# Kernel tuning notes

Measured on AMD Instinct MI355X. Metric: run time of the kernel, lower is better.

The kernel has to match this reference:

```python
import jax, jax.numpy as jnp
import numpy as np

N_NODES = 50000


def _degree_norm(src, dst, n):
    # symmetric GCN normalization with self-loops already appended
    deg = jax.ops.segment_sum(jnp.ones(src.shape[0], jnp.float32), dst, num_segments=n)
    dinv = jnp.where(deg > 0, jax.lax.rsqrt(deg), 0.0)
    return dinv[src] * dinv[dst]  # [E_full]


def _gcn_layer(x, W, b, src, dst, norm, n):
    h = x @ W                                  # [N, out]
    msgs = h[src] * norm[:, None]              # gather + scale, [E_full, out]
    out = jax.ops.segment_sum(msgs, dst, num_segments=n)
    return out + b


def setup_inputs() -> dict:
    key = jax.random.key(0)
    k1, k2, k3, k4 = jax.random.split(key, 4)
    n, e, d_in, d_out = N_NODES, 800000, 256, 128
    x = jax.random.normal(k1, (n, d_in), jnp.float32)
    edge_index = jax.random.randint(k2, (2, e), 0, n, dtype=jnp.int64)
    W1 = jax.random.normal(k3, (d_in, 2 * d_out), jnp.float32) / np.sqrt(d_in)
    b1 = jnp.zeros((2 * d_out,), jnp.float32)
    W2 = jax.random.normal(k4, (2 * d_out, d_out), jnp.float32) / np.sqrt(2 * d_out)
    b2 = jnp.zeros((d_out,), jnp.float32)
    return {"x": x, "edge_index": edge_index, "W1": W1, "b1": b1, "W2": W2, "b2": b2}


def reference(x, edge_index, W1, b1, W2, b2):
    n = x.shape[0]
    loops = jnp.arange(n, dtype=edge_index.dtype)
    src = jnp.concatenate([edge_index[0], loops])
    dst = jnp.concatenate([edge_index[1], loops])
    norm = _degree_norm(src, dst, n)
    h = jax.nn.relu(_gcn_layer(x, W1, b1, src, dst, norm, n))
    h = jax.nn.relu(_gcn_layer(h, W2, b2, src, dst, norm, n))
    return h
```

## Files before the change

kernel.cpp:

```cpp
#include <hip/hip_runtime.h>
#include <hip/hip_bf16.h>


typedef __attribute__((ext_vector_type(8))) short bf16x8;
typedef __attribute__((ext_vector_type(4))) float f32x4;

__device__ inline float bf2f(unsigned short u) {
    return __uint_as_float(((unsigned)u) << 16);
}
__device__ inline unsigned short f2bf(float f) {
    unsigned x = __float_as_uint(f);
    unsigned r = (x + 0x7fffu + ((x >> 16) & 1u)) >> 16;
    return (unsigned short)r;
}
__device__ inline float bflo(unsigned u) { return __uint_as_float(u << 16); }
__device__ inline float bfhi(unsigned u) { return __uint_as_float(u & 0xffff0000u); }

__global__ void degree_kernel(const int* __restrict__ dst, unsigned* __restrict__ deg, int E) {
    int e = blockIdx.x * blockDim.x + threadIdx.x;
    if (e < E) atomicAdd(&deg[dst[e]], 1u);
}

__global__ void dinv_kernel(const unsigned* __restrict__ deg, float* __restrict__ dinv, int N) {
    int i = blockIdx.x * blockDim.x + threadIdx.x;
    if (i < N) dinv[i] = rsqrtf((float)(deg[i] + 1u));
}

__global__ __launch_bounds__(1024) void scan_kernel(const unsigned* __restrict__ deg,
                                                    int* __restrict__ rowptr,
                                                    int* __restrict__ cursor, int N) {
    __shared__ int wsum[16];
    __shared__ int carry_s;
    const int t = threadIdx.x, lane = t & 63, w = t >> 6;
    if (t == 0) carry_s = 0;
    __syncthreads();
    for (int base = 0; base < N; base += 4096) {
        int i0 = base + t * 4;
        int v[4];
#pragma unroll
        for (int j = 0; j < 4; j++) {
            int i = i0 + j;
            v[j] = (i < N) ? (int)deg[i] : 0;
        }
        int s = v[0] + v[1] + v[2] + v[3];
        int x = s;
#pragma unroll
        for (int off = 1; off < 64; off <<= 1) {
            int y = __shfl_up(x, off, 64);
            if (lane >= off) x += y;
        }
        if (lane == 63) wsum[w] = x;
        __syncthreads();
        if (w == 0 && lane < 16) {
            int ss = wsum[lane];
#pragma unroll
            for (int off = 1; off < 16; off <<= 1) {
                int y = __shfl_up(ss, off, 16);
                if ((lane & 15) >= off) ss += y;
            }
            wsum[lane] = ss;
        }
        __syncthreads();
        int waveoff = (w == 0) ? 0 : wsum[w - 1];
        int c = carry_s;
        int run = c + waveoff + (x - s);
#pragma unroll
        for (int j = 0; j < 4; j++) {
            int i = i0 + j;
            if (i < N) { rowptr[i] = run; cursor[i] = run; }
            run += v[j];
        }
        __syncthreads();
        if (t == 1023) carry_s = c + waveoff + x;
        __syncthreads();
    }
    if (t == 0) rowptr[N] = carry_s;
}

__global__ __launch_bounds__(256) void fill_kernel(const int* __restrict__ src,
                                                   const int* __restrict__ dst,
                                                   const float* __restrict__ dinv,
                                                   int* __restrict__ cursor,
                                                   int* __restrict__ col,
                                                   float* __restrict__ wgt, int E) {
    int e = blockIdx.x * blockDim.x + threadIdx.x;
    if (e < E) {
        int d = dst[e];
        int s = src[e];
        int pos = atomicAdd(&cursor[d], 1);
        col[pos] = s;
        wgt[pos] = dinv[s] * dinv[d];
    }
}

__global__ __launch_bounds__(256) void convert_x_kernel(const float* __restrict__ in,
                                                        unsigned short* __restrict__ out,
                                                        long n4) {
    long i = (long)blockIdx.x * blockDim.x + threadIdx.x;
    if (i < n4) {
        float4 v = ((const float4*)in)[i];
        ushort4 o;
        o.x = f2bf(v.x); o.y = f2bf(v.y); o.z = f2bf(v.z); o.w = f2bf(v.w);
        ((ushort4*)out)[i] = o;
    }
}

__global__ __launch_bounds__(256) void convert_wt_kernel(const float* __restrict__ W,
                                                         unsigned short* __restrict__ WT,
                                                         int K, int Nw) {
    int id = blockIdx.x * blockDim.x + threadIdx.x;
    if (id < K * Nw) {
        int k = id / Nw;
        int n = id % Nw;
        WT[(long)n * K + k] = f2bf(W[id]);
    }
}

#define GBM 128
#define GBN 128
#define GBK 64
__global__ __launch_bounds__(256) void gemm_bf16(const unsigned short* __restrict__ A,
                                                 const unsigned short* __restrict__ BT,
                                                 unsigned short* __restrict__ C,
                                                 int M, int Nc, int K) {
    __shared__ __align__(16) unsigned short As[GBM * GBK];
    __shared__ __align__(16) unsigned short Bs[GBN * GBK];
    const int t = threadIdx.x;
    const int lane = t & 63;
    const int w = t >> 6;
    const int row0 = blockIdx.x * GBM;
    const int col0 = blockIdx.y * GBN;
    const int rb = (w >> 1) * 64;
    const int cb = (w & 1) * 64;

    f32x4 acc[4][4] = {};

    for (int kb = 0; kb < K; kb += GBK) {
#pragma unroll
        for (int i = 0; i < 4; i++) {
            int p = i * 256 + t;
            int row = p >> 3;
            int slot = p & 7;
            int chunk = slot ^ (row & 7);
            int grow = row0 + row;
            if (grow >= M) grow = M - 1;
            const unsigned short* src = A + (size_t)grow * K + kb + chunk * 8;
            __builtin_amdgcn_global_load_lds(
                (const __attribute__((address_space(1))) void*)src,
                (__attribute__((address_space(3))) void*)&As[p * 8], 16, 0, 0);
        }
#pragma unroll
        for (int i = 0; i < 4; i++) {
            int p = i * 256 + t;
            int row = p >> 3;
            int slot = p & 7;
            int chunk = slot ^ (row & 7);
            const unsigned short* src = BT + (size_t)(col0 + row) * K + kb + chunk * 8;
            __builtin_amdgcn_global_load_lds(
                (const __attribute__((address_space(1))) void*)src,
                (__attribute__((address_space(3))) void*)&Bs[p * 8], 16, 0, 0);
        }
        asm volatile("s_waitcnt vmcnt(0)" ::: "memory");
        __syncthreads();

#pragma unroll
        for (int ks = 0; ks < 2; ks++) {
            int kq = ks * 4 + (lane >> 4);
            int rsel = lane & 15;
            bf16x8 af[4], bfr[4];
#pragma unroll
            for (int mt = 0; mt < 4; mt++) {
                int m = rb + mt * 16 + rsel;
                int slot = kq ^ (m & 7);
                af[mt] = *(const bf16x8*)&As[m * GBK + slot * 8];
            }
#pragma unroll
            for (int nt = 0; nt < 4; nt++) {
                int n = cb + nt * 16 + rsel;
                int slot = kq ^ (n & 7);
                bfr[nt] = *(const bf16x8*)&Bs[n * GBK + slot * 8];
            }
#pragma unroll
            for (int mt = 0; mt < 4; mt++)
#pragma unroll
                for (int nt = 0; nt < 4; nt++)
                    acc[mt][nt] = __builtin_amdgcn_mfma_f32_16x16x32_bf16(
                        af[mt], bfr[nt], acc[mt][nt], 0, 0, 0);
        }
        __syncthreads();
    }

#pragma unroll
    for (int mt = 0; mt < 4; mt++) {
#pragma unroll
        for (int nt = 0; nt < 4; nt++) {
            int gcol = col0 + cb + nt * 16 + (lane & 15);
            int grow0 = row0 + rb + mt * 16 + 4 * (lane >> 4);
#pragma unroll
            for (int r = 0; r < 4; r++) {
                int g = grow0 + r;
                if (g < M) C[(size_t)g * Nc + gcol] = f2bf(acc[mt][nt][r]);
            }
        }
    }
}

template <int VPL, bool OUT_BF16>
__global__ __launch_bounds__(256) void gather_v2(const unsigned short* __restrict__ h,
                                                 const int* __restrict__ rowptr,
                                                 const int* __restrict__ col,
                                                 const float* __restrict__ wgt,
                                                 const float* __restrict__ dinv,
                                                 const float* __restrict__ bias,
                                                 void* __restrict__ out,
                                                 int N) {
    constexpr int F = VPL * 64;
    const int wv = threadIdx.x >> 6;
    const int lane = threadIdx.x & 63;
    const int node = blockIdx.x * 4 + wv;
    if (node >= N) return;
    const int f0 = lane * VPL;

    const int beg = __builtin_amdgcn_readfirstlane(rowptr[node]);
    const int end = __builtin_amdgcn_readfirstlane(rowptr[node + 1]);

    float a[VPL];
#pragma unroll
    for (int k = 0; k < VPL; k++) a[k] = 0.f;

    int e = beg;
    for (; e + 8 <= end; e += 8) {
        int s[8]; float wvv[8];
#pragma unroll
        for (int j = 0; j < 8; j++) { s[j] = col[e + j]; wvv[j] = wgt[e + j]; }
        if (VPL == 4) {
            uint2 u[8];
#pragma unroll
            for (int j = 0; j < 8; j++)
                u[j] = *(const uint2*)&h[(size_t)s[j] * F + f0];
#pragma unroll
            for (int j = 0; j < 8; j++) {
                a[0] += bflo(u[j].x) * wvv[j];
                a[1] += bfhi(u[j].x) * wvv[j];
                a[2] += bflo(u[j].y) * wvv[j];
                a[3] += bfhi(u[j].y) * wvv[j];
            }
        } else {
            unsigned u[8];
#pragma unroll
            for (int j = 0; j < 8; j++)
                u[j] = *(const unsigned*)&h[(size_t)s[j] * F + f0];
#pragma unroll
            for (int j = 0; j < 8; j++) {
                a[0] += bflo(u[j]) * wvv[j];
                a[1] += bfhi(u[j]) * wvv[j];
            }
        }
    }
    if (e + 4 <= end) {
        int s[4]; float wvv[4];
#pragma unroll
        for (int j = 0; j < 4; j++) { s[j] = col[e + j]; wvv[j] = wgt[e + j]; }
        if (VPL == 4) {
            uint2 u[4];
#pragma unroll
            for (int j = 0; j < 4; j++)
                u[j] = *(const uint2*)&h[(size_t)s[j] * F + f0];
#pragma unroll
            for (int j = 0; j < 4; j++) {
                a[0] += bflo(u[j].x) * wvv[j];
                a[1] += bfhi(u[j].x) * wvv[j];
                a[2] += bflo(u[j].y) * wvv[j];
                a[3] += bfhi(u[j].y) * wvv[j];
            }
        } else {
            unsigned u[4];
#pragma unroll
            for (int j = 0; j < 4; j++)
                u[j] = *(const unsigned*)&h[(size_t)s[j] * F + f0];
#pragma unroll
            for (int j = 0; j < 4; j++) {
                a[0] += bflo(u[j]) * wvv[j];
                a[1] += bfhi(u[j]) * wvv[j];
            }
        }
        e += 4;
    }
    for (; e < end; e++) {
        int s = col[e];
        float wvv = wgt[e];
        if (VPL == 4) {
            uint2 u = *(const uint2*)&h[(size_t)s * F + f0];
            a[0] += bflo(u.x) * wvv;
            a[1] += bfhi(u.x) * wvv;
            a[2] += bflo(u.y) * wvv;
            a[3] += bfhi(u.y) * wvv;
        } else {
            unsigned u = *(const unsigned*)&h[(size_t)s * F + f0];
            a[0] += bflo(u) * wvv;
            a[1] += bfhi(u) * wvv;
        }
    }

    float di = dinv[node];
    float sl = di * di;
    if (VPL == 4) {
        uint2 u = *(const uint2*)&h[(size_t)node * F + f0];
        float4 bv = *(const float4*)&bias[f0];
        float v0 = fmaxf(a[0] + bflo(u.x) * sl + bv.x, 0.f);
        float v1 = fmaxf(a[1] + bfhi(u.x) * sl + bv.y, 0.f);
        float v2 = fmaxf(a[2] + bflo(u.y) * sl + bv.z, 0.f);
        float v3 = fmaxf(a[3] + bfhi(u.y) * sl + bv.w, 0.f);
        if (OUT_BF16) {
            ushort4 o;
            o.x = f2bf(v0); o.y = f2bf(v1); o.z = f2bf(v2); o.w = f2bf(v3);
            *(ushort4*)&((unsigned short*)out)[(size_t)node * F + f0] = o;
        } else {
            float4 o = {v0, v1, v2, v3};
            *(float4*)&((float*)out)[(size_t)node * F + f0] = o;
        }
    } else {
        unsigned u = *(const unsigned*)&h[(size_t)node * F + f0];
        float2 bv = *(const float2*)&bias[f0];
        float v0 = fmaxf(a[0] + bflo(u) * sl + bv.x, 0.f);
        float v1 = fmaxf(a[1] + bfhi(u) * sl + bv.y, 0.f);
        if (OUT_BF16) {
            ushort2 o;
            o.x = f2bf(v0); o.y = f2bf(v1);
            *(ushort2*)&((unsigned short*)out)[(size_t)node * F + f0] = o;
        } else {
            float2 o = {v0, v1};
            *(float2*)&((float*)out)[(size_t)node * F + f0] = o;
        }
    }
}

extern "C" void kernel_launch(void* const* d_in, const int* in_sizes, int n_in,
                              void* d_out, int out_size, void* d_ws, size_t ws_size,
                              hipStream_t stream) {
    const float* x  = (const float*)d_in[0];
    const int* ei   = (const int*)d_in[1];
    const float* W1 = (const float*)d_in[2];
    const float* b1 = (const float*)d_in[3];
    const float* W2 = (const float*)d_in[4];
    const float* b2 = (const float*)d_in[5];

    const int DIN = 256;
    const int N = in_sizes[0] / DIN;
    const int E = in_sizes[1] / 2;
    const int H = in_sizes[3];
    const int DOUT = in_sizes[5];

    const int* src = ei;
    const int* dst = ei + E;

    char* ws = (char*)d_ws;
    unsigned* deg = (unsigned*)ws;                   ws += (size_t)N * 4;
    float* dinv   = (float*)ws;                      ws += (size_t)N * 4;
    int* rowptr   = (int*)ws;                        ws += (size_t)(N + 4) * 4;
    int* cursor   = (int*)ws;                        ws += (size_t)N * 4;
    int* col      = (int*)ws;                        ws += (size_t)E * 4;
    float* wgt    = (float*)ws;                      ws += (size_t)E * 4;
    unsigned short* xb  = (unsigned short*)ws;       ws += (size_t)N * DIN * 2;
    unsigned short* w1t = (unsigned short*)ws;       ws += (size_t)DIN * H * 2;
    unsigned short* w2t = (unsigned short*)ws;       ws += (size_t)H * DOUT * 2;
    unsigned short* h1b = (unsigned short*)ws;       ws += (size_t)N * H * 2;
    unsigned short* y1b = (unsigned short*)ws;       ws += (size_t)N * H * 2;
    unsigned short* h2b = xb;
    float* outp = (float*)d_out;

    hipMemsetAsync(deg, 0, (size_t)N * 4, stream);
    degree_kernel<<<(E + 255) / 256, 256, 0, stream>>>(dst, deg, E);
    dinv_kernel<<<(N + 255) / 256, 256, 0, stream>>>(deg, dinv, N);
    scan_kernel<<<1, 1024, 0, stream>>>(deg, rowptr, cursor, N);
    fill_kernel<<<(E + 255) / 256, 256, 0, stream>>>(src, dst, dinv, cursor, col, wgt, E);

    {
        long n4 = (long)N * DIN / 4;
        convert_x_kernel<<<(int)((n4 + 255) / 256), 256, 0, stream>>>(x, xb, n4);
        convert_wt_kernel<<<(DIN * H + 255) / 256, 256, 0, stream>>>(W1, w1t, DIN, H);
        convert_wt_kernel<<<(H * DOUT + 255) / 256, 256, 0, stream>>>(W2, w2t, H, DOUT);
    }

    {
        dim3 grid((N + GBM - 1) / GBM, H / GBN);
        gemm_bf16<<<grid, 256, 0, stream>>>(xb, w1t, h1b, N, H, DIN);
    }
    gather_v2<4, true><<<(N + 3) / 4, 256, 0, stream>>>(h1b, rowptr, col, wgt, dinv, b1, y1b, N);

    {
        dim3 grid((N + GBM - 1) / GBM, DOUT / GBN);
        gemm_bf16<<<grid, 256, 0, stream>>>(y1b, w2t, h2b, N, DOUT, H);
    }
    gather_v2<2, false><<<(N + 3) / 4, 256, 0, stream>>>(h2b, rowptr, col, wgt, dinv, b2, outp, N);
}
```

Measured before the change: 381.9 us.

## Factor GCN edge norm into GEMM row scale and post-gather scale, shrink col to u16

Removes the per-edge weight array by pre-scaling GEMM output rows with dinv[src] and scaling the aggregated sum by dinv[dst] in the gather. Column indices are stored as 16-bit values, halving index traffic, which only works while node count fits in 16 bits. The dinv computation is folded into the single-block scan kernel, removing one launch. Rounding changes slightly because scaling now happens before bf16 conversion.

```diff
diff --git a/kernel.cpp b/kernel.cpp
--- a/kernel.cpp
+++ b/kernel.cpp
@@ -5,9 +5,6 @@
 typedef __attribute__((ext_vector_type(8))) short bf16x8;
 typedef __attribute__((ext_vector_type(4))) float f32x4;
 
-__device__ inline float bf2f(unsigned short u) {
-    return __uint_as_float(((unsigned)u) << 16);
-}
 __device__ inline unsigned short f2bf(float f) {
     unsigned x = __float_as_uint(f);
     unsigned r = (x + 0x7fffu + ((x >> 16) & 1u)) >> 16;
@@ -21,14 +18,10 @@
     if (e < E) atomicAdd(&deg[dst[e]], 1u);
 }
 
-__global__ void dinv_kernel(const unsigned* __restrict__ deg, float* __restrict__ dinv, int N) {
-    int i = blockIdx.x * blockDim.x + threadIdx.x;
-    if (i < N) dinv[i] = rsqrtf((float)(deg[i] + 1u));
-}
-
 __global__ __launch_bounds__(1024) void scan_kernel(const unsigned* __restrict__ deg,
                                                     int* __restrict__ rowptr,
-                                                    int* __restrict__ cursor, int N) {
+                                                    int* __restrict__ cursor,
+                                                    float* __restrict__ dinv, int N) {
     __shared__ int wsum[16];
     __shared__ int carry_s;
     const int t = threadIdx.x, lane = t & 63, w = t >> 6;
@@ -67,7 +60,11 @@
 #pragma unroll
         for (int j = 0; j < 4; j++) {
             int i = i0 + j;
-            if (i < N) { rowptr[i] = run; cursor[i] = run; }
+            if (i < N) {
+                rowptr[i] = run;
+                cursor[i] = run;
+                dinv[i] = rsqrtf((float)(v[j] + 1));
+            }
             run += v[j];
         }
         __syncthreads();
@@ -79,17 +76,14 @@
 
 __global__ __launch_bounds__(256) void fill_kernel(const int* __restrict__ src,
                                                    const int* __restrict__ dst,
-                                                   const float* __restrict__ dinv,
                                                    int* __restrict__ cursor,
-                                                   int* __restrict__ col,
-                                                   float* __restrict__ wgt, int E) {
+                                                   unsigned short* __restrict__ col, int E) {
     int e = blockIdx.x * blockDim.x + threadIdx.x;
     if (e < E) {
         int d = dst[e];
         int s = src[e];
         int pos = atomicAdd(&cursor[d], 1);
-        col[pos] = s;
-        wgt[pos] = dinv[s] * dinv[d];
+        col[pos] = (unsigned short)s;
     }
 }
 
@@ -122,6 +116,7 @@
 __global__ __launch_bounds__(256) void gemm_bf16(const unsigned short* __restrict__ A,
                                                  const unsigned short* __restrict__ BT,
                                                  unsigned short* __restrict__ C,
+                                                 const float* __restrict__ rowscale,
                                                  int M, int Nc, int K) {
     __shared__ __align__(16) unsigned short As[GBM * GBK];
     __shared__ __align__(16) unsigned short Bs[GBN * GBK];
@@ -199,17 +194,16 @@
 #pragma unroll
             for (int r = 0; r < 4; r++) {
                 int g = grow0 + r;
-                if (g < M) C[(size_t)g * Nc + gcol] = f2bf(acc[mt][nt][r]);
+                if (g < M) C[(size_t)g * Nc + gcol] = f2bf(acc[mt][nt][r] * rowscale[g]);
             }
         }
     }
 }
 
 template <int VPL, bool OUT_BF16>
-__global__ __launch_bounds__(256) void gather_v2(const unsigned short* __restrict__ h,
+__global__ __launch_bounds__(256) void gather_v3(const unsigned short* __restrict__ h,
                                                  const int* __restrict__ rowptr,
-                                                 const int* __restrict__ col,
-                                                 const float* __restrict__ wgt,
+                                                 const unsigned short* __restrict__ col,
                                                  const float* __restrict__ dinv,
                                                  const float* __restrict__ bias,
                                                  void* __restrict__ out,
@@ -230,9 +224,9 @@
 
     int e = beg;
     for (; e + 8 <= end; e += 8) {
-        int s[8]; float wvv[8];
-#pragma unroll
-        for (int j = 0; j < 8; j++) { s[j] = col[e + j]; wvv[j] = wgt[e + j]; }
+        int s[8];
+#pragma unroll
+        for (int j = 0; j < 8; j++) s[j] = col[e + j];
         if (VPL == 4) {
             uint2 u[8];
 #pragma unroll
@@ -240,10 +234,10 @@
                 u[j] = *(const uint2*)&h[(size_t)s[j] * F + f0];
 #pragma unroll
             for (int j = 0; j < 8; j++) {
-                a[0] += bflo(u[j].x) * wvv[j];
-                a[1] += bfhi(u[j].x) * wvv[j];
-                a[2] += bflo(u[j].y) * wvv[j];
-                a[3] += bfhi(u[j].y) * wvv[j];
+                a[0] += bflo(u[j].x);
+                a[1] += bfhi(u[j].x);
+                a[2] += bflo(u[j].y);
+                a[3] += bfhi(u[j].y);
             }
         } else {
             unsigned u[8];
@@ -252,15 +246,15 @@
                 u[j] = *(const unsigned*)&h[(size_t)s[j] * F + f0];
 #pragma unroll
             for (int j = 0; j < 8; j++) {
-                a[0] += bflo(u[j]) * wvv[j];
-                a[1] += bfhi(u[j]) * wvv[j];
+                a[0] += bflo(u[j]);
+                a[1] += bfhi(u[j]);
             }
         }
     }
     if (e + 4 <= end) {
-        int s[4]; float wvv[4];
-#pragma unroll
-        for (int j = 0; j < 4; j++) { s[j] = col[e + j]; wvv[j] = wgt[e + j]; }
+        int s[4];
+#pragma unroll
+        for (int j = 0; j < 4; j++) s[j] = col[e + j];
         if (VPL == 4) {
             uint2 u[4];
 #pragma unroll
@@ -268,10 +262,10 @@
                 u[j] = *(const uint2*)&h[(size_t)s[j] * F + f0];
 #pragma unroll
             for (int j = 0; j < 4; j++) {
-                a[0] += bflo(u[j].x) * wvv[j];
-                a[1] += bfhi(u[j].x) * wvv[j];
-                a[2] += bflo(u[j].y) * wvv[j];
-                a[3] += bfhi(u[j].y) * wvv[j];
+                a[0] += bflo(u[j].x);
+                a[1] += bfhi(u[j].x);
+                a[2] += bflo(u[j].y);
+                a[3] += bfhi(u[j].y);
             }
         } else {
             unsigned u[4];
@@ -280,37 +274,35 @@
                 u[j] = *(const unsigned*)&h[(size_t)s[j] * F + f0];
 #pragma unroll
             for (int j = 0; j < 4; j++) {
-                a[0] += bflo(u[j]) * wvv[j];
-                a[1] += bfhi(u[j]) * wvv[j];
+                a[0] += bflo(u[j]);
+                a[1] += bfhi(u[j]);
             }
         }
         e += 4;
     }
     for (; e < end; e++) {
         int s = col[e];
-        float wvv = wgt[e];
         if (VPL == 4) {
             uint2 u = *(const uint2*)&h[(size_t)s * F + f0];
-            a[0] += bflo(u.x) * wvv;
-            a[1] += bfhi(u.x) * wvv;
-            a[2] += bflo(u.y) * wvv;
-            a[3] += bfhi(u.y) * wvv;
+            a[0] += bflo(u.x);
+            a[1] += bfhi(u.x);
+            a[2] += bflo(u.y);
+            a[3] += bfhi(u.y);
         } else {
             unsigned u = *(const unsigned*)&h[(size_t)s * F + f0];
-            a[0] += bflo(u) * wvv;
-            a[1] += bfhi(u) * wvv;
+            a[0] += bflo(u);
+            a[1] += bfhi(u);
         }
     }
 
     float di = dinv[node];
-    float sl = di * di;
     if (VPL == 4) {
         uint2 u = *(const uint2*)&h[(size_t)node * F + f0];
         float4 bv = *(const float4*)&bias[f0];
-        float v0 = fmaxf(a[0] + bflo(u.x) * sl + bv.x, 0.f);
-        float v1 = fmaxf(a[1] + bfhi(u.x) * sl + bv.y, 0.f);
-        float v2 = fmaxf(a[2] + bflo(u.y) * sl + bv.z, 0.f);
-        float v3 = fmaxf(a[3] + bfhi(u.y) * sl + bv.w, 0.f);
+        float v0 = fmaxf((a[0] + bflo(u.x)) * di + bv.x, 0.f);
+        float v1 = fmaxf((a[1] + bfhi(u.x)) * di + bv.y, 0.f);
+        float v2 = fmaxf((a[2] + bflo(u.y)) * di + bv.z, 0.f);
+        float v3 = fmaxf((a[3] + bfhi(u.y)) * di + bv.w, 0.f);
         if (OUT_BF16) {
             ushort4 o;
             o.x = f2bf(v0); o.y = f2bf(v1); o.z = f2bf(v2); o.w = f2bf(v3);
@@ -322,8 +314,8 @@
     } else {
         unsigned u = *(const unsigned*)&h[(size_t)node * F + f0];
         float2 bv = *(const float2*)&bias[f0];
-        float v0 = fmaxf(a[0] + bflo(u) * sl + bv.x, 0.f);
-        float v1 = fmaxf(a[1] + bfhi(u) * sl + bv.y, 0.f);
+        float v0 = fmaxf((a[0] + bflo(u)) * di + bv.x, 0.f);
+        float v1 = fmaxf((a[1] + bfhi(u)) * di + bv.y, 0.f);
         if (OUT_BF16) {
             ushort2 o;
             o.x = f2bf(v0); o.y = f2bf(v1);
@@ -359,8 +351,7 @@
     float* dinv   = (float*)ws;                      ws += (size_t)N * 4;
     int* rowptr   = (int*)ws;                        ws += (size_t)(N + 4) * 4;
     int* cursor   = (int*)ws;                        ws += (size_t)N * 4;
-    int* col      = (int*)ws;                        ws += (size_t)E * 4;
-    float* wgt    = (float*)ws;                      ws += (size_t)E * 4;
+    unsigned short* col = (unsigned short*)ws;       ws += (size_t)E * 2;
     unsigned short* xb  = (unsigned short*)ws;       ws += (size_t)N * DIN * 2;
     unsigned short* w1t = (unsigned short*)ws;       ws += (size_t)DIN * H * 2;
     unsigned short* w2t = (unsigned short*)ws;       ws += (size_t)H * DOUT * 2;
@@ -371,9 +362,8 @@
 
     hipMemsetAsync(deg, 0, (size_t)N * 4, stream);
     degree_kernel<<<(E + 255) / 256, 256, 0, stream>>>(dst, deg, E);
-    dinv_kernel<<<(N + 255) / 256, 256, 0, stream>>>(deg, dinv, N);
-    scan_kernel<<<1, 1024, 0, stream>>>(deg, rowptr, cursor, N);
-    fill_kernel<<<(E + 255) / 256, 256, 0, stream>>>(src, dst, dinv, cursor, col, wgt, E);
+    scan_kernel<<<1, 1024, 0, stream>>>(deg, rowptr, cursor, dinv, N);
+    fill_kernel<<<(E + 255) / 256, 256, 0, stream>>>(src, dst, cursor, col, E);
 
     {
         long n4 = (long)N * DIN / 4;
@@ -384,13 +374,13 @@
 
     {
         dim3 grid((N + GBM - 1) / GBM, H / GBN);
-        gemm_bf16<<<grid, 256, 0, stream>>>(xb, w1t, h1b, N, H, DIN);
-    }
-    gather_v2<4, true><<<(N + 3) / 4, 256, 0, stream>>>(h1b, rowptr, col, wgt, dinv, b1, y1b, N);
+        gemm_bf16<<<grid, 256, 0, stream>>>(xb, w1t, h1b, dinv, N, H, DIN);
+    }
+    gather_v3<4, true><<<(N + 3) / 4, 256, 0, stream>>>(h1b, rowptr, col, dinv, b1, y1b, N);
 
     {
         dim3 grid((N + GBM - 1) / GBM, DOUT / GBN);
-        gemm_bf16<<<grid, 256, 0, stream>>>(y1b, w2t, h2b, N, DOUT, H);
-    }
-    gather_v2<2, false><<<(N + 3) / 4, 256, 0, stream>>>(h2b, rowptr, col, wgt, dinv, b2, outp, N);
-}
+        gemm_bf16<<<grid, 256, 0, stream>>>(y1b, w2t, h2b, dinv, N, DOUT, H);
+    }
+    gather_v3<2, false><<<(N + 3) / 4, 256, 0, stream>>>(h2b, rowptr, col, dinv, b2, outp, N);
+}
```

New measurement: 409.4 us. 7.2% more time.
